# Performance work log

Hardware: AMD Instinct MI355X
Metric: run time of the kernel (lower is better)

The kernel has to match this reference:

```python
import jax, jax.numpy as jnp
import numpy as np

SIGMA_INIT = 0.0025
EPSILON = 1e-06
B = 8388608


def setup_inputs() -> dict:
    key = jax.random.key(0)
    k1, k2 = jax.random.split(key)
    predictions = jax.random.normal(k1, (B, 3), dtype=jnp.float32)
    targets = jax.random.normal(k2, (B, 3), dtype=jnp.float32)
    sigma = jnp.eye(3, dtype=jnp.float32) * SIGMA_INIT + EPSILON * jnp.eye(3, dtype=jnp.float32)
    return {"predictions": predictions, "targets": targets, "sigma": sigma}


def reference(predictions, targets, sigma):
    sigma_inv = jnp.linalg.inv(sigma)
    sign, log_det_sigma = jnp.linalg.slogdet(sigma)
    # logdet of SPD matrix: sign == 1, so sign*log_det == torch.logdet
    diff = predictions - targets  # [B, 3]
    # vectorized batched quadratic form: diff^T Sigma^{-1} diff per sample
    mahalanobis = jnp.einsum('bi,ij,bj->b', diff, sigma_inv, diff)
    loss = jnp.abs(log_det_sigma + jnp.mean(mahalanobis))
    return loss
```

## Files before the change

kernel.cpp:

```cpp
#include <hip/hip_runtime.h>
#include <math.h>

typedef float f4 __attribute__((ext_vector_type(4)));

#define NBLOCKS 2048
#define NTHREADS 256

__global__ __launch_bounds__(NTHREADS) void moments_kernel(
    const f4* __restrict__ pred, const f4* __restrict__ targ,
    float* __restrict__ partials, int ngroups)
{
    float m00 = 0.f, m01 = 0.f, m02 = 0.f, m11 = 0.f, m12 = 0.f, m22 = 0.f;

    const int stride = gridDim.x * blockDim.x;
    for (int g = blockIdx.x * blockDim.x + threadIdx.x; g < ngroups; g += stride) {
        const long long base = 3LL * (long long)g;
        f4 p0 = pred[base + 0], p1 = pred[base + 1], p2 = pred[base + 2];
        f4 t0 = targ[base + 0], t1 = targ[base + 1], t2 = targ[base + 2];
        f4 d0 = p0 - t0, d1 = p1 - t1, d2 = p2 - t2;

        float xs[4] = { d0.x, d0.w, d1.z, d2.y };
        float ys[4] = { d0.y, d1.x, d1.w, d2.z };
        float zs[4] = { d0.z, d1.y, d2.x, d2.w };
#pragma unroll
        for (int s = 0; s < 4; ++s) {
            float x = xs[s], y = ys[s], z = zs[s];
            m00 += x * x; m11 += y * y; m22 += z * z;
            m01 += x * y; m02 += x * z; m12 += y * z;
        }
    }

    float acc[6] = { m00, m01, m02, m11, m12, m22 };
#pragma unroll
    for (int off = 32; off > 0; off >>= 1) {
#pragma unroll
        for (int k = 0; k < 6; ++k) acc[k] += __shfl_down(acc[k], off, 64);
    }

    __shared__ float sm[4][6];
    const int wave = threadIdx.x >> 6;
    const int lane = threadIdx.x & 63;
    if (lane == 0) {
#pragma unroll
        for (int k = 0; k < 6; ++k) sm[wave][k] = acc[k];
    }
    __syncthreads();
    if (threadIdx.x == 0) {
#pragma unroll
        for (int k = 0; k < 6; ++k)
            partials[blockIdx.x * 6 + k] = sm[0][k] + sm[1][k] + sm[2][k] + sm[3][k];
    }
}

__global__ __launch_bounds__(NTHREADS) void finalize_kernel(
    const float* __restrict__ partials, const float* __restrict__ sigma,
    const float* __restrict__ pred, const float* __restrict__ targ,
    float* __restrict__ out, int nblocks, int tail_start, int n)
{
    double a[6] = { 0, 0, 0, 0, 0, 0 };
    for (int b = threadIdx.x; b < nblocks; b += blockDim.x) {
#pragma unroll
        for (int k = 0; k < 6; ++k) a[k] += (double)partials[b * 6 + k];
    }
#pragma unroll
    for (int off = 32; off > 0; off >>= 1) {
#pragma unroll
        for (int k = 0; k < 6; ++k) a[k] += __shfl_down(a[k], off, 64);
    }

    __shared__ double sm[4][6];
    const int wave = threadIdx.x >> 6;
    const int lane = threadIdx.x & 63;
    if (lane == 0) {
#pragma unroll
        for (int k = 0; k < 6; ++k) sm[wave][k] = a[k];
    }
    __syncthreads();

    if (threadIdx.x == 0) {
        double M[6];
#pragma unroll
        for (int k = 0; k < 6; ++k) M[k] = sm[0][k] + sm[1][k] + sm[2][k] + sm[3][k];

        for (int i = tail_start; i < n; ++i) {
            double x = (double)pred[3 * i + 0] - (double)targ[3 * i + 0];
            double y = (double)pred[3 * i + 1] - (double)targ[3 * i + 1];
            double z = (double)pred[3 * i + 2] - (double)targ[3 * i + 2];
            M[0] += x * x; M[1] += x * y; M[2] += x * z;
            M[3] += y * y; M[4] += y * z; M[5] += z * z;
        }

        const double invN = 1.0 / (double)n;
#pragma unroll
        for (int k = 0; k < 6; ++k) M[k] *= invN;

        double s00 = sigma[0], s01 = sigma[1], s02 = sigma[2];
        double s10 = sigma[3], s11 = sigma[4], s12 = sigma[5];
        double s20 = sigma[6], s21 = sigma[7], s22 = sigma[8];

        double c00 = s11 * s22 - s12 * s21;
        double c01 = s12 * s20 - s10 * s22;
        double c02 = s10 * s21 - s11 * s20;
        double det = s00 * c00 + s01 * c01 + s02 * c02;
        double invdet = 1.0 / det;

        double i00 = (s11 * s22 - s12 * s21) * invdet;
        double i01 = (s02 * s21 - s01 * s22) * invdet;
        double i02 = (s01 * s12 - s02 * s11) * invdet;
        double i10 = (s12 * s20 - s10 * s22) * invdet;
        double i11 = (s00 * s22 - s02 * s20) * invdet;
        double i12 = (s02 * s10 - s00 * s12) * invdet;
        double i20 = (s10 * s21 - s11 * s20) * invdet;
        double i21 = (s01 * s20 - s00 * s21) * invdet;
        double i22 = (s00 * s11 - s01 * s10) * invdet;

        double quad = i00 * M[0] + i11 * M[3] + i22 * M[5]
                    + (i01 + i10) * M[1] + (i02 + i20) * M[2] + (i12 + i21) * M[4];

        double logdet = log(fabs(det));
        out[0] = (float)fabs(logdet + quad);
    }
}

extern "C" void kernel_launch(void* const* d_in, const int* in_sizes, int n_in,
                              void* d_out, int out_size, void* d_ws, size_t ws_size,
                              hipStream_t stream) {
    const float* pred  = (const float*)d_in[0];
    const float* targ  = (const float*)d_in[1];
    const float* sigma = (const float*)d_in[2];
    float* out = (float*)d_out;

    const int n = in_sizes[0] / 3;
    const int ngroups = n / 4;
    const int tail_start = ngroups * 4;

    float* partials = (float*)d_ws;

    moments_kernel<<<NBLOCKS, NTHREADS, 0, stream>>>(
        (const f4*)pred, (const f4*)targ, partials, ngroups);
    finalize_kernel<<<1, NTHREADS, 0, stream>>>(
        partials, sigma, pred, targ, out, NBLOCKS, tail_start, n);
}
```

Baseline: 38.83 us.

## Coalesce global loads via LDS transpose of diff tiles

Each block now loads a tile of 768 float4s with unit stride across threads, so neighbouring lanes read contiguous memory instead of stride-3 float4s. The differences are staged in LDS with a padded layout and read back so each thread gets its 3-float4 group. This targets the poor coalescing of the strided loads, at the cost of two barriers per tile and extra LDS traffic.

After: 39.46 us. No clear change (+1.6%).

```diff
diff --git a/kernel.cpp b/kernel.cpp
--- a/kernel.cpp
+++ b/kernel.cpp
@@ -5,26 +5,46 @@
 
 #define NBLOCKS 2048
 #define NTHREADS 256
+#define TILE_F4 768
+#define CS 259
 
 __global__ __launch_bounds__(NTHREADS) void moments_kernel(
     const f4* __restrict__ pred, const f4* __restrict__ targ,
-    float* __restrict__ partials, int ngroups)
+    float* __restrict__ partials, int ntiles)
 {
+    __shared__ f4 lds[3 * CS];
+
+    const int t = threadIdx.x;
+
+    int widx[3];
+#pragma unroll
+    for (int k = 0; k < 3; ++k) {
+        const int j = k * NTHREADS + t;
+        widx[k] = (j % 3) * CS + (j / 3);
+    }
+    const int r0 = 0 * CS + t, r1 = 1 * CS + t, r2 = 2 * CS + t;
+
     float m00 = 0.f, m01 = 0.f, m02 = 0.f, m11 = 0.f, m12 = 0.f, m22 = 0.f;
 
-    const int stride = gridDim.x * blockDim.x;
-    for (int g = blockIdx.x * blockDim.x + threadIdx.x; g < ngroups; g += stride) {
-        const long long base = 3LL * (long long)g;
-        f4 p0 = pred[base + 0], p1 = pred[base + 1], p2 = pred[base + 2];
-        f4 t0 = targ[base + 0], t1 = targ[base + 1], t2 = targ[base + 2];
-        f4 d0 = p0 - t0, d1 = p1 - t1, d2 = p2 - t2;
+    for (int T = blockIdx.x; T < ntiles; T += gridDim.x) {
+        const long long base = (long long)T * TILE_F4 + t;
+        f4 p0 = pred[base], p1 = pred[base + 256], p2 = pred[base + 512];
+        f4 q0 = targ[base], q1 = targ[base + 256], q2 = targ[base + 512];
 
-        float xs[4] = { d0.x, d0.w, d1.z, d2.y };
-        float ys[4] = { d0.y, d1.x, d1.w, d2.z };
-        float zs[4] = { d0.z, d1.y, d2.x, d2.w };
+        lds[widx[0]] = p0 - q0;
+        lds[widx[1]] = p1 - q1;
+        lds[widx[2]] = p2 - q2;
+        __syncthreads();
+
+        f4 a = lds[r0], b = lds[r1], c = lds[r2];
+        __syncthreads();
+
+        float xs[4] = { a.x, a.w, b.z, c.y };
+        float ys[4] = { a.y, b.x, b.w, c.z };
+        float zs[4] = { a.z, b.y, c.x, c.w };
 #pragma unroll
         for (int s = 0; s < 4; ++s) {
-            float x = xs[s], y = ys[s], z = zs[s];
+            const float x = xs[s], y = ys[s], z = zs[s];
             m00 += x * x; m11 += y * y; m22 += z * z;
             m01 += x * y; m02 += x * z; m12 += y * z;
         }
@@ -38,14 +58,14 @@
     }
 
     __shared__ float sm[4][6];
-    const int wave = threadIdx.x >> 6;
-    const int lane = threadIdx.x & 63;
+    const int wave = t >> 6;
+    const int lane = t & 63;
     if (lane == 0) {
 #pragma unroll
         for (int k = 0; k < 6; ++k) sm[wave][k] = acc[k];
     }
     __syncthreads();
-    if (threadIdx.x == 0) {
+    if (t == 0) {
 #pragma unroll
         for (int k = 0; k < 6; ++k)
             partials[blockIdx.x * 6 + k] = sm[0][k] + sm[1][k] + sm[2][k] + sm[3][k];
@@ -131,13 +151,14 @@
     float* out = (float*)d_out;
 
     const int n = in_sizes[0] / 3;
-    const int ngroups = n / 4;
-    const int tail_start = ngroups * 4;
+    const int nf4 = in_sizes[0] / 4;
+    const int ntiles = nf4 / TILE_F4;
+    const int tail_start = (ntiles * TILE_F4 * 4) / 3;
 
     float* partials = (float*)d_ws;
 
     moments_kernel<<<NBLOCKS, NTHREADS, 0, stream>>>(
-        (const f4*)pred, (const f4*)targ, partials, ngroups);
+        (const f4*)pred, (const f4*)targ, partials, ntiles);
     finalize_kernel<<<1, NTHREADS, 0, stream>>>(
         partials, sigma, pred, targ, out, NBLOCKS, tail_start, n);
 }
```

## Fuse finalize into moments kernel via last-block atomic counter, 8 samples per thread

Applied to the files above, without the earlier changes.

Merges the two-kernel reduction into one kernel: each block writes its partial moments, increments a global atomic counter, and the last block to arrive does the final double-precision reduction and loss computation. This removes the second kernel launch and its dependency gap, but adds a hipMemsetAsync to reset the counter on every call. The per-thread work is also doubled to 8 samples (six float4 loads per input) per loop iteration to increase memory-level parallelism.

New measurement: 107.5 us. 177% more time.

```diff
diff --git a/kernel.cpp b/kernel.cpp
--- a/kernel.cpp
+++ b/kernel.cpp
@@ -6,25 +6,31 @@
 #define NBLOCKS 2048
 #define NTHREADS 256
 
-__global__ __launch_bounds__(NTHREADS) void moments_kernel(
-    const f4* __restrict__ pred, const f4* __restrict__ targ,
-    float* __restrict__ partials, int ngroups)
+__global__ __launch_bounds__(NTHREADS) void fused_kernel(
+    const f4* __restrict__ pred4, const f4* __restrict__ targ4,
+    const float* __restrict__ sigma,
+    const float* __restrict__ predf, const float* __restrict__ targf,
+    float* __restrict__ partials, unsigned int* __restrict__ counter,
+    float* __restrict__ out, int ngroups8, int tail_start, int n)
 {
     float m00 = 0.f, m01 = 0.f, m02 = 0.f, m11 = 0.f, m12 = 0.f, m22 = 0.f;
 
     const int stride = gridDim.x * blockDim.x;
-    for (int g = blockIdx.x * blockDim.x + threadIdx.x; g < ngroups; g += stride) {
-        const long long base = 3LL * (long long)g;
-        f4 p0 = pred[base + 0], p1 = pred[base + 1], p2 = pred[base + 2];
-        f4 t0 = targ[base + 0], t1 = targ[base + 1], t2 = targ[base + 2];
-        f4 d0 = p0 - t0, d1 = p1 - t1, d2 = p2 - t2;
+    for (int g = blockIdx.x * blockDim.x + threadIdx.x; g < ngroups8; g += stride) {
+        const long long base = 6LL * (long long)g;
+        f4 p0 = pred4[base + 0], p1 = pred4[base + 1], p2 = pred4[base + 2];
+        f4 p3 = pred4[base + 3], p4 = pred4[base + 4], p5 = pred4[base + 5];
+        f4 q0 = targ4[base + 0], q1 = targ4[base + 1], q2 = targ4[base + 2];
+        f4 q3 = targ4[base + 3], q4 = targ4[base + 4], q5 = targ4[base + 5];
+        f4 d0 = p0 - q0, d1 = p1 - q1, d2 = p2 - q2;
+        f4 d3 = p3 - q3, d4 = p4 - q4, d5 = p5 - q5;
 
-        float xs[4] = { d0.x, d0.w, d1.z, d2.y };
-        float ys[4] = { d0.y, d1.x, d1.w, d2.z };
-        float zs[4] = { d0.z, d1.y, d2.x, d2.w };
+        float xs[8] = { d0.x, d0.w, d1.z, d2.y, d3.x, d3.w, d4.z, d5.y };
+        float ys[8] = { d0.y, d1.x, d1.w, d2.z, d3.y, d4.x, d4.w, d5.z };
+        float zs[8] = { d0.z, d1.y, d2.x, d2.w, d3.z, d4.y, d5.x, d5.w };
 #pragma unroll
-        for (int s = 0; s < 4; ++s) {
-            float x = xs[s], y = ys[s], z = zs[s];
+        for (int s = 0; s < 8; ++s) {
+            const float x = xs[s], y = ys[s], z = zs[s];
             m00 += x * x; m11 += y * y; m22 += z * z;
             m01 += x * y; m02 += x * z; m12 += y * z;
         }
@@ -37,28 +43,31 @@
         for (int k = 0; k < 6; ++k) acc[k] += __shfl_down(acc[k], off, 64);
     }
 
-    __shared__ float sm[4][6];
+    __shared__ float smf[4][6];
+    __shared__ bool amLast;
     const int wave = threadIdx.x >> 6;
     const int lane = threadIdx.x & 63;
     if (lane == 0) {
 #pragma unroll
-        for (int k = 0; k < 6; ++k) sm[wave][k] = acc[k];
+        for (int k = 0; k < 6; ++k) smf[wave][k] = acc[k];
     }
     __syncthreads();
+
     if (threadIdx.x == 0) {
 #pragma unroll
         for (int k = 0; k < 6; ++k)
-            partials[blockIdx.x * 6 + k] = sm[0][k] + sm[1][k] + sm[2][k] + sm[3][k];
+            partials[blockIdx.x * 6 + k] = smf[0][k] + smf[1][k] + smf[2][k] + smf[3][k];
+        __threadfence();
+        unsigned int old = atomicAdd(counter, 1u);
+        amLast = (old == gridDim.x - 1);
     }
-}
+    __syncthreads();
+    if (!amLast) return;
 
-__global__ __launch_bounds__(NTHREADS) void finalize_kernel(
-    const float* __restrict__ partials, const float* __restrict__ sigma,
-    const float* __restrict__ pred, const float* __restrict__ targ,
-    float* __restrict__ out, int nblocks, int tail_start, int n)
-{
+    __threadfence();
+
     double a[6] = { 0, 0, 0, 0, 0, 0 };
-    for (int b = threadIdx.x; b < nblocks; b += blockDim.x) {
+    for (int b = threadIdx.x; b < NBLOCKS; b += NTHREADS) {
 #pragma unroll
         for (int k = 0; k < 6; ++k) a[k] += (double)partials[b * 6 + k];
     }
@@ -68,24 +77,22 @@
         for (int k = 0; k < 6; ++k) a[k] += __shfl_down(a[k], off, 64);
     }
 
-    __shared__ double sm[4][6];
-    const int wave = threadIdx.x >> 6;
-    const int lane = threadIdx.x & 63;
+    __shared__ double smd[4][6];
     if (lane == 0) {
 #pragma unroll
-        for (int k = 0; k < 6; ++k) sm[wave][k] = a[k];
+        for (int k = 0; k < 6; ++k) smd[wave][k] = a[k];
     }
     __syncthreads();
 
     if (threadIdx.x == 0) {
         double M[6];
 #pragma unroll
-        for (int k = 0; k < 6; ++k) M[k] = sm[0][k] + sm[1][k] + sm[2][k] + sm[3][k];
+        for (int k = 0; k < 6; ++k) M[k] = smd[0][k] + smd[1][k] + smd[2][k] + smd[3][k];
 
         for (int i = tail_start; i < n; ++i) {
-            double x = (double)pred[3 * i + 0] - (double)targ[3 * i + 0];
-            double y = (double)pred[3 * i + 1] - (double)targ[3 * i + 1];
-            double z = (double)pred[3 * i + 2] - (double)targ[3 * i + 2];
+            double x = (double)predf[3 * i + 0] - (double)targf[3 * i + 0];
+            double y = (double)predf[3 * i + 1] - (double)targf[3 * i + 1];
+            double z = (double)predf[3 * i + 2] - (double)targf[3 * i + 2];
             M[0] += x * x; M[1] += x * y; M[2] += x * z;
             M[3] += y * y; M[4] += y * z; M[5] += z * z;
         }
@@ -131,13 +138,16 @@
     float* out = (float*)d_out;
 
     const int n = in_sizes[0] / 3;
-    const int ngroups = n / 4;
-    const int tail_start = ngroups * 4;
+    const int ngroups8 = n / 8;
+    const int tail_start = ngroups8 * 8;
 
     float* partials = (float*)d_ws;
+    unsigned int* counter =
+        (unsigned int*)((char*)d_ws + NBLOCKS * 6 * sizeof(float));
 
-    moments_kernel<<<NBLOCKS, NTHREADS, 0, stream>>>(
-        (const f4*)pred, (const f4*)targ, partials, ngroups);
-    finalize_kernel<<<1, NTHREADS, 0, stream>>>(
-        partials, sigma, pred, targ, out, NBLOCKS, tail_start, n);
+    hipMemsetAsync(counter, 0, sizeof(unsigned int), stream);
+
+    fused_kernel<<<NBLOCKS, NTHREADS, 0, stream>>>(
+        (const f4*)pred, (const f4*)targ, sigma, pred, targ,
+        partials, counter, out, ngroups8, tail_start, n);
 }
```
